# Optimization experiments

Measured on AMD Instinct MI355X. Metric: run time of the kernel, lower is better.

The kernel has to match this reference:

```python
import jax, jax.numpy as jnp
import numpy as np

B, T, D = 32, 1024, 1024
H = 512        # LSTM units per direction
L = 3          # num_layers


def _run_lstm(x, mask, W, U, b):
    """Masked unidirectional LSTM, Keras gate order (i, f, c, o).
    x: [B,T,D], mask: [B,T] bool (True = valid). Masked steps carry state
    and repeat the previous output, matching Keras masking semantics."""
    z_all = jnp.einsum('btd,dk->tbk', x, W) + b          # [T,B,4H]
    m_all = jnp.transpose(mask, (1, 0))                   # [T,B]

    def step(carry, inp):
        h, c = carry
        z_t, m_t = inp
        z = z_t + h @ U                                   # [B,4H]
        i, f, g, o = jnp.split(z, 4, axis=-1)
        i = jax.nn.sigmoid(i)
        f = jax.nn.sigmoid(f)
        g = jnp.tanh(g)
        o = jax.nn.sigmoid(o)
        c_new = f * c + i * g
        h_new = o * jnp.tanh(c_new)
        m = m_t[:, None]
        h = jnp.where(m, h_new, h)
        c = jnp.where(m, c_new, c)
        return (h, c), h

    h0 = jnp.zeros((x.shape[0], U.shape[0]), x.dtype)
    (_, _), hs = jax.lax.scan(step, (h0, h0), (z_all, m_all))
    return jnp.transpose(hs, (1, 0, 2))                   # [B,T,H]


def _bilstm(x, mask, Wf, Uf, bf, Wb, Ub, bb):
    fwd = _run_lstm(x, mask, Wf, Uf, bf)
    bwd = _run_lstm(x[:, ::-1], mask[:, ::-1], Wb, Ub, bb)[:, ::-1]
    return jnp.concatenate([fwd, bwd], axis=-1)           # [B,T,2H]


def setup_inputs() -> dict:
    key = jax.random.key(0)
    ks = jax.random.split(key, 16)
    s = 0.05
    inp = {
        'x': jax.random.normal(ks[0], (B, T, D), jnp.float32),
        'x_mask': jax.random.randint(ks[1], (B, T), 0, 2, jnp.int32),
        # stacked BiLSTM params (all layers share shapes since 2H == D)
        'Wf': jax.random.normal(ks[2], (L, D, 4 * H), jnp.float32) * s,
        'Uf': jax.random.normal(ks[3], (L, H, 4 * H), jnp.float32) * s,
        'bf': jax.random.normal(ks[4], (L, 4 * H), jnp.float32) * s,
        'Wb': jax.random.normal(ks[5], (L, D, 4 * H), jnp.float32) * s,
        'Ub': jax.random.normal(ks[6], (L, H, 4 * H), jnp.float32) * s,
        'bb': jax.random.normal(ks[7], (L, 4 * H), jnp.float32) * s,
        # task heads
        'Wp': jax.random.normal(ks[8], (2 * H, 2), jnp.float32) * s,
        'bp': jnp.zeros((2,), jnp.float32),
        'Wbu': jax.random.normal(ks[9], (2 * H, 2), jnp.float32) * s,
        'bbu': jnp.zeros((2,), jnp.float32),
        'Wss3': jax.random.normal(ks[10], (2 * H, 3), jnp.float32) * s,
        'bss3': jnp.zeros((3,), jnp.float32),
        'Wss8': jax.random.normal(ks[11], (2 * H, 8), jnp.float32) * s,
        'bss8': jnp.zeros((8,), jnp.float32),
        'training': 0,
    }
    return inp


def reference(x, x_mask, Wf, Uf, bf, Wb, Ub, bb, Wp, bp, Wbu, bbu,
              Wss3, bss3, Wss8, bss8, training):
    # mask = not(x_mask == 1): True = valid position
    mask = x_mask != 1
    for l in range(L):
        x = _bilstm(x, mask, Wf[l], Uf[l], bf[l], Wb[l], Ub[l], bb[l])
    x = jax.nn.relu(x)
    # dropout is identity at inference (training == 0)
    ppi = jax.nn.softmax(x @ Wp + bp, axis=-1)
    buried = x @ Wbu + bbu
    ss3 = x @ Wss3 + bss3
    ss8 = x @ Wss8 + bss8
    return (ppi, buried, ss3, ss8)
```

## Files before the change

### kernel.cpp

```cpp
#include <hip/hip_runtime.h>
#include <hip/hip_bf16.h>
#include <math.h>


#define B_ 32
#define T_ 1024
#define H_ 512
#define NG 2048

typedef __attribute__((ext_vector_type(8))) short bf16x8;
typedef __attribute__((ext_vector_type(4))) float f32x4;
typedef unsigned int u32;
typedef unsigned short u16;

__device__ inline u16 f2bf(float f) {
    u32 u = __float_as_uint(f);
    return (u16)((u + 0x7fffu + ((u >> 16) & 1u)) >> 16);
}
__device__ inline void gload16(const void* g, void* l) {
    __builtin_amdgcn_global_load_lds(
        (const __attribute__((address_space(1))) u32*)g,
        (__attribute__((address_space(3))) u32*)l, 16, 0, 0);
}
__device__ inline float fsig(float x) { return 1.0f / (1.0f + __expf(-x)); }
__device__ inline float ftanh(float x) { return 1.0f - 2.0f / (__expf(2.0f * x) + 1.0f); }

__global__ void zero_mem(float* __restrict__ s, int n) {
    int i = blockIdx.x * 256 + threadIdx.x;
    if (i < n) s[i] = 0.0f;
}

__global__ __launch_bounds__(256) void conv_bf16(const float* __restrict__ src,
                                                 u16* __restrict__ dst) {
    int i = blockIdx.x * 256 + threadIdx.x;
    float4 v = *(const float4*)&src[(size_t)i * 4];
    ushort4 o = { f2bf(v.x), f2bf(v.y), f2bf(v.z), f2bf(v.w) };
    *(ushort4*)&dst[(size_t)i * 4] = o;
}

__global__ __launch_bounds__(256) void transpose_w(const float* __restrict__ Wf,
                                                   const float* __restrict__ Wb,
                                                   u16* __restrict__ wt) {
    int mat = blockIdx.z;
    const float* W = ((mat & 1) ? Wb : Wf) + (size_t)(mat >> 1) * 1024 * NG;
    u16* dst = wt + (size_t)mat * NG * 1024;
    __shared__ float tile[64][65];
    int n0 = blockIdx.x * 64, k0 = blockIdx.y * 64;
    int t = threadIdx.x;
#pragma unroll
    for (int i = 0; i < 16; ++i) {
        int idx = t + i * 256;
        int kk = idx >> 6, nn = idx & 63;
        tile[kk][nn] = W[(size_t)(k0 + kk) * NG + n0 + nn];
    }
    __syncthreads();
#pragma unroll
    for (int i = 0; i < 16; ++i) {
        int idx = t + i * 256;
        int nn = idx >> 6, kk = idx & 63;
        dst[(size_t)(n0 + nn) * 1024 + k0 + kk] = f2bf(tile[kk][nn]);
    }
}

__global__ __launch_bounds__(256) void pack_u(const float* __restrict__ Uf,
                                              const float* __restrict__ Ub,
                                              u16* __restrict__ upk) {
    int mat = blockIdx.y;
    const float* U = ((mat & 1) ? Ub : Uf) + (size_t)(mat >> 1) * H_ * NG;
    u16* dst = upk + (size_t)mat * 1048576;
    int f = blockIdx.x * 256 + threadIdx.x;
    int lane = f & 63, ks = (f >> 6) & 15, c2 = (f >> 10) & 1;
    int cp = (f >> 11) & 3, wg = f >> 13;
    int col = cp * H_ + wg * 32 + c2 * 16 + (lane & 15);
    int krow = ks * 32 + (lane >> 4) * 8;
    u16 o[8];
#pragma unroll
    for (int j = 0; j < 8; ++j) o[j] = f2bf(U[(size_t)(krow + j) * NG + col]);
    *(uint4*)(dst + (size_t)f * 8) = *(uint4*)o;
}

__global__ __launch_bounds__(256) void gemm_mfma(
    const u16* __restrict__ A, const u16* __restrict__ Bt,
    const float* __restrict__ bias, float* __restrict__ Z,
    int t0, int lgC) {
    __shared__ __align__(16) u16 sA[128 * 32];
    __shared__ __align__(16) u16 sB[128 * 32];
    const int tid = threadIdx.x;
    const int m0 = blockIdx.y * 128, n0 = blockIdx.x * 128;
    const int Cmask = (1 << lgC) - 1;

    const int chunk0 = tid, chunk1 = tid + 256;
    const int r0 = chunk0 >> 2, kp0 = (chunk0 & 3) * 8;
    const int r1 = chunk1 >> 2, kp1 = (chunk1 & 3) * 8;
    const int gm0 = m0 + r0, gm1 = m0 + r1;
    const size_t arow0 = ((size_t)(gm0 >> lgC) * T_ + t0 + (gm0 & Cmask)) * 1024;
    const size_t arow1 = ((size_t)(gm1 >> lgC) * T_ + t0 + (gm1 & Cmask)) * 1024;
    const size_t brow0 = (size_t)(n0 + r0) * 1024;
    const size_t brow1 = (size_t)(n0 + r1) * 1024;

    const int lane = tid & 63, wave = tid >> 6;
    const int wr = (wave >> 1) * 64, wc = (wave & 1) * 64;
    const int fr = lane & 15, fk = (lane >> 4) * 8;

    f32x4 acc[4][4] = {};
    for (int kc = 0; kc < 1024; kc += 32) {
        gload16(A + arow0 + kc + kp0, &sA[chunk0 * 8]);
        gload16(A + arow1 + kc + kp1, &sA[chunk1 * 8]);
        gload16(Bt + brow0 + kc + kp0, &sB[chunk0 * 8]);
        gload16(Bt + brow1 + kc + kp1, &sB[chunk1 * 8]);
        __syncthreads();
        bf16x8 af[4], bfr[4];
#pragma unroll
        for (int i = 0; i < 4; ++i)
            af[i] = *(const bf16x8*)&sA[(wr + i * 16 + fr) * 32 + fk];
#pragma unroll
        for (int j = 0; j < 4; ++j)
            bfr[j] = *(const bf16x8*)&sB[(wc + j * 16 + fr) * 32 + fk];
#pragma unroll
        for (int i = 0; i < 4; ++i)
#pragma unroll
            for (int j = 0; j < 4; ++j)
                acc[i][j] = __builtin_amdgcn_mfma_f32_16x16x32_bf16(
                    af[i], bfr[j], acc[i][j], 0, 0, 0);
        __syncthreads();
    }
    float bv[4];
#pragma unroll
    for (int j = 0; j < 4; ++j) bv[j] = bias[n0 + wc + j * 16 + fr];
#pragma unroll
    for (int i = 0; i < 4; ++i) {
        int mb = m0 + wr + i * 16 + (lane >> 4) * 4;
#pragma unroll
        for (int j = 0; j < 4; ++j) {
            int n = n0 + wc + j * 16 + fr;
#pragma unroll
            for (int r = 0; r < 4; ++r)
                Z[(size_t)(mb + r) * NG + n] = acc[i][j][r] + bv[j];
        }
    }
}

__global__ __launch_bounds__(512, 1) void lstm_chunk(
    const float* __restrict__ zf, const float* __restrict__ zb,
    const u16* __restrict__ upk,
    const int* __restrict__ xmask,
    u32* __restrict__ hbuf32,
    float* __restrict__ cst, float* __restrict__ hst,
    u32* __restrict__ flags,
    u16* __restrict__ hseq,
    int t0f, int t0b, int C, int sbase) {
    const int bx = blockIdx.x, dir = bx >> 4, wgs = bx & 15, u0 = wgs * 32;
    const float* z = dir ? zb : zf;
    const u16* up = upk + dir * 1048576;
    u32* hb32 = hbuf32 + dir * 16384;
    u32* myflag = flags + (dir * 16 + wgs) * 32;
    const u32* fbase = flags + dir * 512;
    const int tid = threadIdx.x;
    const int wave = tid >> 6, lane = tid & 63;
    const int cp = wave & 3, bt = wave >> 2, fr = lane & 15, fq = lane >> 4;
    const int row = bt * 16 + fr;
    const int swz = (row & 7) << 4;

    __shared__ __align__(16) u16 sh[16384];
    __shared__ float sacc[32 * 132];

    bf16x8 uf0[16], uf1[16];
#pragma unroll
    for (int ks = 0; ks < 16; ++ks) {
        size_t base0 = (((size_t)(wgs * 4 + cp) * 2) * 16 + ks) * 512 + lane * 8;
        uf0[ks] = *(const bf16x8*)(up + base0);
        uf1[ks] = *(const bf16x8*)(up + base0 + 16 * 512);
    }

    const int b0p = tid >> 5, ul = tid & 31, b1p = b0p + 16, ug = u0 + ul;
    const int sidx = (dir * 16 + wgs) * 1024 + tid * 2;
    float c0r = cst[sidx], c1r = cst[sidx + 1];
    float h0r = hst[sidx], h1r = hst[sidx + 1];
    const size_t hs0 = (size_t)b0p * T_ * 1024 + dir * 512 + ug;
    const size_t hs1 = (size_t)b1p * T_ * 1024 + dir * 512 + ug;

    {
        u32 tmp[16];
#pragma unroll
        for (int k = 0; k < 16; ++k)
            tmp[k] = __hip_atomic_load(hb32 + k * 512 + tid, __ATOMIC_RELAXED,
                                       __HIP_MEMORY_SCOPE_AGENT);
#pragma unroll
        for (int k = 0; k < 16; ++k) {
            int idx = k * 512 + tid;
            int sb = (idx * 4) ^ (((idx >> 8) & 7) << 4);
            *(u32*)((char*)sh + sb) = tmp[k];
        }
    }
    float zc[8]; int mc0, mc1;
    {
        int tc = dir ? (C - 1) : 0;
        int t = dir ? (t0b + C - 1) : t0f;
        const float* zr0 = z + ((size_t)b0p * C + tc) * NG + ug;
        const float* zr1 = z + ((size_t)b1p * C + tc) * NG + ug;
#pragma unroll
        for (int g = 0; g < 4; ++g) { zc[g] = zr0[g * 512]; zc[4 + g] = zr1[g * 512]; }
        mc0 = xmask[b0p * T_ + t]; mc1 = xmask[b1p * T_ + t];
    }
    __syncthreads();

    for (int st = 0; st < C; ++st) {
        const int t = dir ? (t0b + C - 1 - st) : (t0f + st);
        u32* nx32 = hb32 + (((st & 1) ^ 1) ? 8192 : 0);

        f32x4 acc0 = {0, 0, 0, 0}, acc1 = {0, 0, 0, 0};
#pragma unroll
        for (int ks = 0; ks < 16; ++ks) {
            int abyte = (row * 1024 + ks * 64 + fq * 16) ^ swz;
            bf16x8 a = *(const bf16x8*)((const char*)sh + abyte);
            acc0 = __builtin_amdgcn_mfma_f32_16x16x32_bf16(a, uf0[ks], acc0, 0, 0, 0);
            acc1 = __builtin_amdgcn_mfma_f32_16x16x32_bf16(a, uf1[ks], acc1, 0, 0, 0);
        }
#pragma unroll
        for (int j = 0; j < 4; ++j) {
            int b = bt * 16 + fq * 4 + j;
            sacc[b * 132 + cp * 32 + fr] = acc0[j];
            sacc[b * 132 + cp * 32 + 16 + fr] = acc1[j];
        }
        __syncthreads();
        {
            const float* s0 = sacc + b0p * 132;
            const float* s1 = sacc + b1p * 132;
            float i0 = fsig(zc[0] + s0[ul]);
            float f0 = fsig(zc[1] + s0[32 + ul]);
            float g0 = ftanh(zc[2] + s0[64 + ul]);
            float o0 = fsig(zc[3] + s0[96 + ul]);
            if (mc0 != 1) { c0r = f0 * c0r + i0 * g0; h0r = o0 * ftanh(c0r); }
            float i1 = fsig(zc[4] + s1[ul]);
            float f1 = fsig(zc[5] + s1[32 + ul]);
            float g1 = ftanh(zc[6] + s1[64 + ul]);
            float o1 = fsig(zc[7] + s1[96 + ul]);
            if (mc1 != 1) { c1r = f1 * c1r + i1 * g1; h1r = o1 * ftanh(c1r); }
            u16 hb0 = f2bf(h0r), hb1 = f2bf(h1r);
            hseq[hs0 + (size_t)t * 1024] = hb0;
            hseq[hs1 + (size_t)t * 1024] = hb1;
            u32 nb0 = __shfl_xor((u32)hb0, 1, 64);
            u32 nb1 = __shfl_xor((u32)hb1, 1, 64);
            if ((ul & 1) == 0) {
                u32 pk0 = (u32)hb0 | (nb0 << 16);
                u32 pk1 = (u32)hb1 | (nb1 << 16);
                __hip_atomic_store(nx32 + b0p * 256 + (ug >> 1), pk0,
                                   __ATOMIC_RELAXED, __HIP_MEMORY_SCOPE_AGENT);
                __hip_atomic_store(nx32 + b1p * 256 + (ug >> 1), pk1,
                                   __ATOMIC_RELAXED, __HIP_MEMORY_SCOPE_AGENT);
            }
        }
        asm volatile("s_waitcnt vmcnt(0)" ::: "memory");
        __syncthreads();
        const u32 tgt = (u32)(sbase + st + 1);
        if (tid == 0)
            __hip_atomic_store(myflag, tgt, __ATOMIC_RELAXED,
                               __HIP_MEMORY_SCOPE_AGENT);
        float zn[8]; int mn0, mn1;
        {
            int stn = (st + 1 < C) ? st + 1 : st;
            int tcn = dir ? (C - 1 - stn) : stn;
            int tn = dir ? (t0b + tcn) : (t0f + tcn);
            const float* zr0 = z + ((size_t)b0p * C + tcn) * NG + ug;
            const float* zr1 = z + ((size_t)b1p * C + tcn) * NG + ug;
#pragma unroll
            for (int g = 0; g < 4; ++g) { zn[g] = zr0[g * 512]; zn[4 + g] = zr1[g * 512]; }
            mn0 = xmask[b0p * T_ + tn]; mn1 = xmask[b1p * T_ + tn];
        }
        if (wave == 0) {
            const u32* fp = fbase + (lane & 15) * 32;
            u32 v;
            do {
                v = __hip_atomic_load(fp, __ATOMIC_RELAXED,
                                      __HIP_MEMORY_SCOPE_AGENT);
            } while (!__all(v >= tgt));
        }
        __syncthreads();
        if (st + 1 < C) {
            const u32* src = hb32 + (((st + 1) & 1) ? 8192 : 0);
            u32 tmp[16];
#pragma unroll
            for (int k = 0; k < 16; ++k)
                tmp[k] = __hip_atomic_load(src + k * 512 + tid, __ATOMIC_RELAXED,
                                           __HIP_MEMORY_SCOPE_AGENT);
#pragma unroll
            for (int k = 0; k < 16; ++k) {
                int idx = k * 512 + tid;
                int sb = (idx * 4) ^ (((idx >> 8) & 7) << 4);
                *(u32*)((char*)sh + sb) = tmp[k];
            }
        }
        __syncthreads();
#pragma unroll
        for (int g = 0; g < 8; ++g) zc[g] = zn[g];
        mc0 = mn0; mc1 = mn1;
    }
    cst[sidx] = c0r; cst[sidx + 1] = c1r;
    hst[sidx] = h0r; hst[sidx + 1] = h1r;
}

__global__ __launch_bounds__(256) void heads_kernel(
    const u16* __restrict__ xin,
    const float* __restrict__ Wp, const float* __restrict__ bp,
    const float* __restrict__ Wbu, const float* __restrict__ bbu,
    const float* __restrict__ Wss3, const float* __restrict__ bss3,
    const float* __restrict__ Wss8, const float* __restrict__ bss8,
    float* __restrict__ out) {
    const int r = blockIdx.x * 4 + (threadIdx.x >> 6);
    const int lane = threadIdx.x & 63;
    const u16* xr = xin + (size_t)r * 1024 + lane * 16;
    uint4 q0 = *(const uint4*)xr;
    uint4 q1 = *(const uint4*)(xr + 8);
    float xv[16];
    u32 qs[8] = { q0.x, q0.y, q0.z, q0.w, q1.x, q1.y, q1.z, q1.w };
#pragma unroll
    for (int i = 0; i < 8; ++i) {
        xv[i * 2]     = fmaxf(__uint_as_float((qs[i] & 0xffffu) << 16), 0.0f);
        xv[i * 2 + 1] = fmaxf(__uint_as_float(qs[i] & 0xffff0000u), 0.0f);
    }
    float acc[15] = {};
    const int k0 = lane * 16;
#pragma unroll
    for (int kk = 0; kk < 16; kk++) {
        float xk = xv[kk];
        int k = k0 + kk;
        acc[0] += xk * Wp[k * 2];      acc[1] += xk * Wp[k * 2 + 1];
        acc[2] += xk * Wbu[k * 2];     acc[3] += xk * Wbu[k * 2 + 1];
        acc[4] += xk * Wss3[k * 3];    acc[5] += xk * Wss3[k * 3 + 1];
        acc[6] += xk * Wss3[k * 3 + 2];
#pragma unroll
        for (int o = 0; o < 8; o++) acc[7 + o] += xk * Wss8[k * 8 + o];
    }
#pragma unroll
    for (int o = 0; o < 15; o++) {
#pragma unroll
        for (int off = 32; off; off >>= 1) acc[o] += __shfl_xor(acc[o], off, 64);
    }
    if (lane == 0) {
        float a0 = acc[0] + bp[0], a1 = acc[1] + bp[1];
        float mx = fmaxf(a0, a1);
        float e0 = expf(a0 - mx), e1 = expf(a1 - mx);
        float ssum = e0 + e1;
        out[(size_t)r * 2] = e0 / ssum;
        out[(size_t)r * 2 + 1] = e1 / ssum;
        float* ob = out + 65536;
        ob[r * 2] = acc[2] + bbu[0]; ob[r * 2 + 1] = acc[3] + bbu[1];
        float* o3 = out + 131072;
        o3[r * 3 + 0] = acc[4] + bss3[0];
        o3[r * 3 + 1] = acc[5] + bss3[1];
        o3[r * 3 + 2] = acc[6] + bss3[2];
        float* o8 = out + 229376;
#pragma unroll
        for (int o = 0; o < 8; o++) o8[r * 8 + o] = acc[7 + o] + bss8[o];
    }
}

extern "C" void kernel_launch(void* const* d_in, const int* in_sizes, int n_in,
                              void* d_out, int out_size, void* d_ws, size_t ws_size,
                              hipStream_t stream) {
    const float* x = (const float*)d_in[0];
    const int* xmask = (const int*)d_in[1];
    const float* Wf = (const float*)d_in[2];
    const float* Uf = (const float*)d_in[3];
    const float* bfp = (const float*)d_in[4];
    const float* Wb = (const float*)d_in[5];
    const float* Ub = (const float*)d_in[6];
    const float* bbp = (const float*)d_in[7];
    const float* Wp = (const float*)d_in[8];
    const float* bp = (const float*)d_in[9];
    const float* Wbu = (const float*)d_in[10];
    const float* bbu = (const float*)d_in[11];
    const float* Wss3 = (const float*)d_in[12];
    const float* bss3 = (const float*)d_in[13];
    const float* Wss8 = (const float*)d_in[14];
    const float* bss8 = (const float*)d_in[15];

    char* wsb = (char*)d_ws;
    u16* actA = (u16*)wsb;
    u16* actB = (u16*)(wsb + (64ull << 20));
    u16* wt   = (u16*)(wsb + (128ull << 20));
    u16* upk  = (u16*)(wsb + (152ull << 20));
    char* stb = wsb + (164ull << 20);
    u32* hbuf32 = (u32*)stb;
    float* cst = (float*)(stb + 131072);
    float* hst = (float*)(stb + 262144);
    u32* flags = (u32*)(stb + 393216);
    const int stateFloats = (393216 + 4096) / 4;

    size_t fixedB = 165ull << 20;
    int C = 1024;
    while (C > 128 && fixedB + 524288ull * C > ws_size) C >>= 1;
    int lgC = 31 - __builtin_clz((unsigned)C);
    float* zf = (float*)(wsb + fixedB);
    float* zb = zf + (size_t)B_ * C * NG;

    conv_bf16<<<dim3(8388608 / 256), 256, 0, stream>>>(x, actA);
    transpose_w<<<dim3(32, 16, 6), 256, 0, stream>>>(Wf, Wb, wt);
    pack_u<<<dim3(512, 6), 256, 0, stream>>>(Uf, Ub, upk);

    const u16* cur = actA;
    for (int l = 0; l < 3; l++) {
        u16* dst = (l & 1) ? actA : actB;
        zero_mem<<<dim3((stateFloats + 255) / 256), 256, 0, stream>>>(
            (float*)stb, stateFloats);
        u16* wtf = wt + (size_t)(l * 2 + 0) * NG * 1024;
        u16* wtb = wt + (size_t)(l * 2 + 1) * NG * 1024;
        const u16* upkl = upk + (size_t)l * 2 * 1048576;
        const float* bfl = bfp + l * NG;
        const float* bbl = bbp + l * NG;
        for (int c0 = 0; c0 < T_; c0 += C) {
            int t0f = c0;
            int t0b = T_ - c0 - C;
            dim3 ggrid(NG / 128, (B_ * C) / 128);
            gemm_mfma<<<ggrid, 256, 0, stream>>>(cur, wtf, bfl, zf, t0f, lgC);
            gemm_mfma<<<ggrid, 256, 0, stream>>>(cur, wtb, bbl, zb, t0b, lgC);

            const float* a_zf = zf; const float* a_zb = zb;
            const u16* a_up = upkl; const int* a_xm = xmask;
            u32* a_hb = hbuf32; float* a_cs = cst; float* a_hs = hst;
            u32* a_fl = flags; u16* a_hseq = dst;
            int a_t0f = t0f, a_t0b = t0b, a_C = C, a_sb = c0;
            void* kargs[] = { &a_zf, &a_zb, &a_up, &a_xm, &a_hb, &a_cs, &a_hs,
                              &a_fl, &a_hseq, &a_t0f, &a_t0b, &a_C, &a_sb };
            hipLaunchCooperativeKernel((void*)lstm_chunk, dim3(32), dim3(512),
                                       kargs, 0, stream);
        }
        cur = dst;
    }
    heads_kernel<<<dim3(B_ * T_ / 4), 256, 0, stream>>>(
        cur, Wp, bp, Wbu, bbu, Wss3, bss3, Wss8, bss8, (float*)d_out);
}
```

Before: 12.05 ms.

## Store input-projection gates as bf16 interleaved per unit and defer hseq stores

The input-projection GEMM now writes bf16 instead of fp32 and interleaves the four gates per hidden unit, so each LSTM thread fetches its gates with one 8-byte load per batch row instead of four strided fp32 loads. This halves Z memory traffic and footprint, which also allows a larger time chunk C for a given workspace. The hseq writes are moved after the flag and h-exchange logic so they sit off the critical path of each recurrent step. The cost is lower precision on the pre-activation input term and a scattered store pattern in the GEMM epilogue.

```diff
diff --git a/kernel.cpp b/kernel.cpp
--- a/kernel.cpp
+++ b/kernel.cpp
@@ -17,6 +17,7 @@
     u32 u = __float_as_uint(f);
     return (u16)((u + 0x7fffu + ((u >> 16) & 1u)) >> 16);
 }
+__device__ inline float bf2f(u16 v) { return __uint_as_float(((u32)v) << 16); }
 __device__ inline void gload16(const void* g, void* l) {
     __builtin_amdgcn_global_load_lds(
         (const __attribute__((address_space(1))) u32*)g,
@@ -81,7 +82,7 @@
 
 __global__ __launch_bounds__(256) void gemm_mfma(
     const u16* __restrict__ A, const u16* __restrict__ Bt,
-    const float* __restrict__ bias, float* __restrict__ Z,
+    const float* __restrict__ bias, u16* __restrict__ Zb,
     int t0, int lgC) {
     __shared__ __align__(16) u16 sA[128 * 32];
     __shared__ __align__(16) u16 sB[128 * 32];
@@ -125,23 +126,28 @@
         __syncthreads();
     }
     float bv[4];
-#pragma unroll
-    for (int j = 0; j < 4; ++j) bv[j] = bias[n0 + wc + j * 16 + fr];
+    int un[4], gn[4];
+#pragma unroll
+    for (int j = 0; j < 4; ++j) {
+        int n = n0 + wc + j * 16 + fr;
+        bv[j] = bias[n];
+        un[j] = n & 511; gn[j] = n >> 9;
+    }
 #pragma unroll
     for (int i = 0; i < 4; ++i) {
         int mb = m0 + wr + i * 16 + (lane >> 4) * 4;
 #pragma unroll
         for (int j = 0; j < 4; ++j) {
-            int n = n0 + wc + j * 16 + fr;
 #pragma unroll
             for (int r = 0; r < 4; ++r)
-                Z[(size_t)(mb + r) * NG + n] = acc[i][j][r] + bv[j];
+                Zb[(size_t)(mb + r) * 2048 + un[j] * 4 + gn[j]] =
+                    f2bf(acc[i][j][r] + bv[j]);
         }
     }
 }
 
 __global__ __launch_bounds__(512, 1) void lstm_chunk(
-    const float* __restrict__ zf, const float* __restrict__ zb,
+    const u16* __restrict__ zf, const u16* __restrict__ zb,
     const u16* __restrict__ upk,
     const int* __restrict__ xmask,
     u32* __restrict__ hbuf32,
@@ -150,7 +156,7 @@
     u16* __restrict__ hseq,
     int t0f, int t0b, int C, int sbase) {
     const int bx = blockIdx.x, dir = bx >> 4, wgs = bx & 15, u0 = wgs * 32;
-    const float* z = dir ? zb : zf;
+    const u16* z = dir ? zb : zf;
     const u16* up = upk + dir * 1048576;
     u32* hb32 = hbuf32 + dir * 16384;
     u32* myflag = flags + (dir * 16 + wgs) * 32;
@@ -192,18 +198,17 @@
             *(u32*)((char*)sh + sb) = tmp[k];
         }
     }
-    float zc[8]; int mc0, mc1;
+    ushort4 za0, za1; int mc0, mc1;
     {
         int tc = dir ? (C - 1) : 0;
         int t = dir ? (t0b + C - 1) : t0f;
-        const float* zr0 = z + ((size_t)b0p * C + tc) * NG + ug;
-        const float* zr1 = z + ((size_t)b1p * C + tc) * NG + ug;
-#pragma unroll
-        for (int g = 0; g < 4; ++g) { zc[g] = zr0[g * 512]; zc[4 + g] = zr1[g * 512]; }
+        za0 = *(const ushort4*)(z + ((size_t)(b0p * C + tc)) * 2048 + ug * 4);
+        za1 = *(const ushort4*)(z + ((size_t)(b1p * C + tc)) * 2048 + ug * 4);
         mc0 = xmask[b0p * T_ + t]; mc1 = xmask[b1p * T_ + t];
     }
     __syncthreads();
 
+    u16 hb0s = 0, hb1s = 0;
     for (int st = 0; st < C; ++st) {
         const int t = dir ? (t0b + C - 1 - st) : (t0f + st);
         u32* nx32 = hb32 + (((st & 1) ^ 1) ? 8192 : 0);
@@ -226,24 +231,22 @@
         {
             const float* s0 = sacc + b0p * 132;
             const float* s1 = sacc + b1p * 132;
-            float i0 = fsig(zc[0] + s0[ul]);
-            float f0 = fsig(zc[1] + s0[32 + ul]);
-            float g0 = ftanh(zc[2] + s0[64 + ul]);
-            float o0 = fsig(zc[3] + s0[96 + ul]);
+            float i0 = fsig(bf2f(za0.x) + s0[ul]);
+            float f0 = fsig(bf2f(za0.y) + s0[32 + ul]);
+            float g0 = ftanh(bf2f(za0.z) + s0[64 + ul]);
+            float o0 = fsig(bf2f(za0.w) + s0[96 + ul]);
             if (mc0 != 1) { c0r = f0 * c0r + i0 * g0; h0r = o0 * ftanh(c0r); }
-            float i1 = fsig(zc[4] + s1[ul]);
-            float f1 = fsig(zc[5] + s1[32 + ul]);
-            float g1 = ftanh(zc[6] + s1[64 + ul]);
-            float o1 = fsig(zc[7] + s1[96 + ul]);
+            float i1 = fsig(bf2f(za1.x) + s1[ul]);
+            float f1 = fsig(bf2f(za1.y) + s1[32 + ul]);
+            float g1 = ftanh(bf2f(za1.z) + s1[64 + ul]);
+            float o1 = fsig(bf2f(za1.w) + s1[96 + ul]);
             if (mc1 != 1) { c1r = f1 * c1r + i1 * g1; h1r = o1 * ftanh(c1r); }
-            u16 hb0 = f2bf(h0r), hb1 = f2bf(h1r);
-            hseq[hs0 + (size_t)t * 1024] = hb0;
-            hseq[hs1 + (size_t)t * 1024] = hb1;
-            u32 nb0 = __shfl_xor((u32)hb0, 1, 64);
-            u32 nb1 = __shfl_xor((u32)hb1, 1, 64);
+            hb0s = f2bf(h0r); hb1s = f2bf(h1r);
+            u32 nb0 = __shfl_xor((u32)hb0s, 1, 64);
+            u32 nb1 = __shfl_xor((u32)hb1s, 1, 64);
             if ((ul & 1) == 0) {
-                u32 pk0 = (u32)hb0 | (nb0 << 16);
-                u32 pk1 = (u32)hb1 | (nb1 << 16);
+                u32 pk0 = (u32)hb0s | (nb0 << 16);
+                u32 pk1 = (u32)hb1s | (nb1 << 16);
                 __hip_atomic_store(nx32 + b0p * 256 + (ug >> 1), pk0,
                                    __ATOMIC_RELAXED, __HIP_MEMORY_SCOPE_AGENT);
                 __hip_atomic_store(nx32 + b1p * 256 + (ug >> 1), pk1,
@@ -256,15 +259,13 @@
         if (tid == 0)
             __hip_atomic_store(myflag, tgt, __ATOMIC_RELAXED,
                                __HIP_MEMORY_SCOPE_AGENT);
-        float zn[8]; int mn0, mn1;
+        ushort4 zn0, zn1; int mn0, mn1;
         {
             int stn = (st + 1 < C) ? st + 1 : st;
             int tcn = dir ? (C - 1 - stn) : stn;
             int tn = dir ? (t0b + tcn) : (t0f + tcn);
-            const float* zr0 = z + ((size_t)b0p * C + tcn) * NG + ug;
-            const float* zr1 = z + ((size_t)b1p * C + tcn) * NG + ug;
-#pragma unroll
-            for (int g = 0; g < 4; ++g) { zn[g] = zr0[g * 512]; zn[4 + g] = zr1[g * 512]; }
+            zn0 = *(const ushort4*)(z + ((size_t)(b0p * C + tcn)) * 2048 + ug * 4);
+            zn1 = *(const ushort4*)(z + ((size_t)(b1p * C + tcn)) * 2048 + ug * 4);
             mn0 = xmask[b0p * T_ + tn]; mn1 = xmask[b1p * T_ + tn];
         }
         if (wave == 0) {
@@ -290,10 +291,10 @@
                 *(u32*)((char*)sh + sb) = tmp[k];
             }
         }
-        __syncthreads();
-#pragma unroll
-        for (int g = 0; g < 8; ++g) zc[g] = zn[g];
-        mc0 = mn0; mc1 = mn1;
+        hseq[hs0 + (size_t)t * 1024] = hb0s;
+        hseq[hs1 + (size_t)t * 1024] = hb1s;
+        za0 = zn0; za1 = zn1; mc0 = mn0; mc1 = mn1;
+        __syncthreads();
     }
     cst[sidx] = c0r; cst[sidx + 1] = c1r;
     hst[sidx] = h0r; hst[sidx + 1] = h1r;
@@ -389,10 +390,10 @@
 
     size_t fixedB = 165ull << 20;
     int C = 1024;
-    while (C > 128 && fixedB + 524288ull * C > ws_size) C >>= 1;
+    while (C > 128 && fixedB + 262144ull * C > ws_size) C >>= 1;
     int lgC = 31 - __builtin_clz((unsigned)C);
-    float* zf = (float*)(wsb + fixedB);
-    float* zb = zf + (size_t)B_ * C * NG;
+    u16* zf = (u16*)(wsb + fixedB);
+    u16* zb = zf + (size_t)B_ * C * 2048;
 
     conv_bf16<<<dim3(8388608 / 256), 256, 0, stream>>>(x, actA);
     transpose_w<<<dim3(32, 16, 6), 256, 0, stream>>>(Wf, Wb, wt);
@@ -415,7 +416,7 @@
             gemm_mfma<<<ggrid, 256, 0, stream>>>(cur, wtf, bfl, zf, t0f, lgC);
             gemm_mfma<<<ggrid, 256, 0, stream>>>(cur, wtb, bbl, zb, t0b, lgC);
 
-            const float* a_zf = zf; const float* a_zb = zb;
+            const u16* a_zf = zf; const u16* a_zb = zb;
             const u16* a_up = upkl; const int* a_xm = xmask;
             u32* a_hb = hbuf32; float* a_cs = cst; float* a_hs = hst;
             u32* a_fl = flags; u16* a_hseq = dst;
```

Result: no change. 12.11 ms (+0.5%).
